# Kernel optimization log

Measured on AMD Instinct MI355X. Metric: run time of the kernel, lower is better.

The kernel has to match this reference:

```python
import jax, jax.numpy as jnp
import numpy as np

EPS = 1e-5  # BatchNorm eps; BN applied in eval mode with running_mean=0, running_var=1


def conv1x1(x, w, b=None):
    # x: [B,C,H,W], w: [O,C] -> [B,O,H,W]
    y = jnp.einsum('bchw,oc->bohw', x, w)
    if b is not None:
        y = y + b[None, :, None, None]
    return y


def bn_eval(x, gamma, beta):
    # running_mean=0, running_var=1
    scale = gamma / jnp.sqrt(1.0 + EPS)
    return x * scale[None, :, None, None] + beta[None, :, None, None]


def glnl_forward(x, mask, wt_nl, bt_nl, wp_nl, bp_nl, wt_l, bt_l, wp_l, bp_l,
                 wg_nl, bg_nl, wg_l, bg_l, wW, bW, gW, betaW, wWl, gWl, betaWl):
    B, C, H, W = x.shape
    I = wt_nl.shape[0]
    N = H * W

    # non-local branch score [B,N,N]
    th_nl = conv1x1(x, wt_nl, bt_nl).reshape(B, I, N)
    ph_nl = conv1x1(x, wp_nl, bp_nl).reshape(B, I, N)
    score_nl = jax.nn.softmax(jnp.einsum('bin,bim->bnm', th_nl, ph_nl), axis=-1)

    # local branch: mask-gated projections, score [B,N,N]
    m = mask.reshape(B, 1, N)
    th_l = conv1x1(x, wt_l, bt_l).reshape(B, I, N) * m
    ph_l = conv1x1(x, wp_l, bp_l).reshape(B, I, N) * m
    score_l = jax.nn.softmax(jnp.einsum('bin,bim->bnm', th_l, ph_l), axis=-1)

    # value projections [B,I,N]
    g_nl = conv1x1(x, wg_nl, bg_nl).reshape(B, I, N)
    g_l = conv1x1(x, wg_l, bg_l).reshape(B, I, N)

    # attention aggregation -> [B,I,H,W]
    y_nl = jnp.einsum('bnm,bim->bin', score_nl, g_nl).reshape(B, I, H, W)
    y_l = jnp.einsum('bnm,bim->bin', score_l, g_l).reshape(B, I, H, W)

    # W_local: conv1x1 (no bias) -> ReLU -> BN
    y_l = bn_eval(jax.nn.relu(conv1x1(y_l, wWl)), gWl, betaWl)

    y = y_nl + y_l
    # W: conv1x1 -> ReLU -> BN, then residual
    W_y = bn_eval(jax.nn.relu(conv1x1(y, wW, bW)), gW, betaW)
    return W_y + x


def setup_inputs() -> dict:
    key = jax.random.key(0)
    ks = jax.random.split(key, 20)
    B, C, I, H, W = 4, 128, 64, 64, 64
    s = 0.02
    inp = {
        'x': jax.random.normal(ks[0], (B, C, H, W), jnp.float32),
        'mask': (jax.random.uniform(ks[1], (B, 1, H, W)) > 0.5).astype(jnp.float32),
        'wt_nl': jax.random.normal(ks[2], (I, C)) * s, 'bt_nl': jnp.zeros((I,)),
        'wp_nl': jax.random.normal(ks[3], (I, C)) * s, 'bp_nl': jnp.zeros((I,)),
        'wt_l': jax.random.normal(ks[4], (I, C)) * s, 'bt_l': jnp.zeros((I,)),
        'wp_l': jax.random.normal(ks[5], (I, C)) * s, 'bp_l': jnp.zeros((I,)),
        'wg_nl': jax.random.normal(ks[6], (I, C)) * s, 'bg_nl': jnp.zeros((I,)),
        'wg_l': jax.random.normal(ks[7], (I, C)) * s, 'bg_l': jnp.zeros((I,)),
        'wW': jax.random.normal(ks[8], (C, I)) * s, 'bW': jnp.zeros((C,)),
        'gW': jnp.ones((C,)), 'betaW': jnp.zeros((C,)),
        'wWl': jax.random.normal(ks[9], (I, I)) * s,
        'gWl': jnp.ones((I,)), 'betaWl': jnp.zeros((I,)),
    }
    return inp


def reference(x, mask, wt_nl, bt_nl, wp_nl, bp_nl, wt_l, bt_l, wp_l, bp_l,
              wg_nl, bg_nl, wg_l, bg_l, wW, bW, gW, betaW, wWl, gWl, betaWl):
    return glnl_forward(x, mask, wt_nl, bt_nl, wp_nl, bp_nl, wt_l, bt_l, wp_l, bp_l,
                        wg_nl, bg_nl, wg_l, bg_l, wW, bW, gW, betaW, wWl, gWl, betaWl)
```

## Files before the change

kernel.cpp:

```cpp
#include <hip/hip_runtime.h>

typedef unsigned short u16;
typedef __attribute__((ext_vector_type(8))) short short8;
typedef __attribute__((ext_vector_type(4))) float floatx4;
typedef __attribute__((ext_vector_type(2))) unsigned int uint2e;

#define MFMA16(a, b, c) __builtin_amdgcn_mfma_f32_16x16x32_bf16((a), (b), (c), 0, 0, 0)
#define LOG2E 1.44269504088896340736f

#define SZ_P ((size_t)4 * 64 * 4096)

__device__ __forceinline__ float bf2f(u16 u) {
    union { unsigned int i; float f; } v; v.i = ((unsigned int)u) << 16; return v.f;
}
__device__ __forceinline__ u16 f2bf(float f) {
    union { float f; unsigned int i; } v; v.f = f;
    unsigned int r = v.i + 0x7fffu + ((v.i >> 16) & 1u);
    return (u16)(r >> 16);
}
__device__ __forceinline__ unsigned int cvtpk(float a, float b) {
    unsigned int r;
    asm("v_cvt_pk_bf16_f32 %0, %1, %2" : "=v"(r) : "v"(a), "v"(b));
    return r;
}
__device__ __forceinline__ void plswap32(unsigned int &a, unsigned int &b) {
#if __has_builtin(__builtin_amdgcn_permlane32_swap)
    uint2e r = __builtin_amdgcn_permlane32_swap(a, b, false, false);
    a = r.x; b = r.y;
#else
    asm volatile("v_permlane32_swap_b32 %0, %1" : "+v"(a), "+v"(b));
#endif
}
__device__ __forceinline__ void plswap16(unsigned int &a, unsigned int &b) {
#if __has_builtin(__builtin_amdgcn_permlane16_swap)
    uint2e r = __builtin_amdgcn_permlane16_swap(a, b, false, false);
    a = r.x; b = r.y;
#else
    asm volatile("v_permlane16_swap_b32 %0, %1" : "+v"(a), "+v"(b));
#endif
}
__device__ __forceinline__ int swz(int row, int g) {
    return row * 64 + (((g ^ (row & 7)) << 3));
}
__device__ __forceinline__ void gload16(const void* g, void* l) {
    __builtin_amdgcn_global_load_lds(
        (const __attribute__((address_space(1))) unsigned char*)g,
        (__attribute__((address_space(3))) unsigned char*)l, 16, 0, 0);
}

__global__ __launch_bounds__(256) void k_prep_w(
    const float* __restrict__ w0, const float* __restrict__ w1,
    const float* __restrict__ w2, const float* __restrict__ w3,
    const float* __restrict__ w4, const float* __restrict__ w5,
    const float* __restrict__ wWl, const float* __restrict__ wW,
    u16* __restrict__ wbf)
{
    const int idx = blockIdx.x * 256 + threadIdx.x;
    float v;
    if (idx < 49152) {
        const int j = idx >> 13, off = idx & 8191;
        const float* s = (j == 0) ? w0 : (j == 1) ? w1 : (j == 2) ? w2
                       : (j == 3) ? w3 : (j == 4) ? w4 : w5;
        v = s[off];
    } else if (idx < 53248) {
        v = wWl[idx - 49152];
    } else {
        v = wW[idx - 53248];
    }
    wbf[idx] = f2bf(v);
}

__global__ __launch_bounds__(256) void k_proj(
    const float* __restrict__ x, const float* __restrict__ mask,
    const u16* __restrict__ wbf,
    const float* __restrict__ bq0f, const float* __restrict__ bk0f,
    const float* __restrict__ bv0f,
    const float* __restrict__ bq1f, const float* __restrict__ bk1f,
    const float* __restrict__ bv1f,
    u16* __restrict__ q0, u16* __restrict__ k0, u16* __restrict__ v0,
    u16* __restrict__ q1, u16* __restrict__ k1, u16* __restrict__ v1)
{
    __shared__ __align__(16) u16 xt_s[64 * 136];
    const int n0 = blockIdx.x * 64, b = blockIdx.y;
    const int br = blockIdx.z;
    const u16* wq = wbf + br * 24576;
    const u16* wk = wq + 8192;
    const u16* wv = wk + 8192;
    const float* bq = br ? bq1f : bq0f;
    const float* bk = br ? bk1f : bk0f;
    const float* bv = br ? bv1f : bv0f;
    u16* q = br ? q1 : q0;  u16* k = br ? k1 : k0;  u16* v = br ? v1 : v0;

    const int t = threadIdx.x, w = t >> 6, lane = t & 63;
    const int quad = lane >> 4, l15 = lane & 15;
    const float* xb = x + ((size_t)b << 19);

    for (int idx = t; idx < 8192; idx += 256) {
        const int c = idx >> 6, n = idx & 63;
        xt_s[n * 136 + c] = f2bf(xb[((size_t)c << 12) + n0 + n]);
    }
    __syncthreads();

    short8 ax[4];
#pragma unroll
    for (int cc = 0; cc < 4; ++cc)
        ax[cc] = *(const short8*)&xt_s[(w * 16 + l15) * 136 + quad * 8 + cc * 32];

    float mv[4] = {1.f, 1.f, 1.f, 1.f};
    if (br) {
#pragma unroll
        for (int r = 0; r < 4; ++r)
            mv[r] = mask[((size_t)b << 12) + n0 + w * 16 + quad * 4 + r];
    }

#pragma unroll
    for (int qk = 0; qk < 2; ++qk) {
        const u16* wsel = qk ? wk : wq;
        const float* bb = qk ? bk : bq;
        u16* o = qk ? k : q;
        const float qscale = qk ? 1.0f : LOG2E;
#pragma unroll
        for (int ns = 0; ns < 4; ++ns) {
            floatx4 acc = {0.f, 0.f, 0.f, 0.f};
            const u16* wp = wsel + (ns * 16 + l15) * 128 + quad * 8;
#pragma unroll
            for (int cc = 0; cc < 4; ++cc)
                acc = MFMA16(ax[cc], *(const short8*)(wp + cc * 32), acc);
            const float bias_i = bb[ns * 16 + l15];
#pragma unroll
            for (int r = 0; r < 4; ++r) {
                const float val = (acc[r] + bias_i) * mv[r] * qscale;
                o[((size_t)b << 18) + (size_t)(n0 + w * 16 + quad * 4 + r) * 64
                  + ns * 16 + l15] = f2bf(val);
            }
        }
    }

    short8 aw[4];
#pragma unroll
    for (int cc = 0; cc < 4; ++cc)
        aw[cc] = *(const short8*)(wv + (w * 16 + l15) * 128 + quad * 8 + cc * 32);
    float bvr[4];
#pragma unroll
    for (int r = 0; r < 4; ++r) bvr[r] = bv[w * 16 + quad * 4 + r];
#pragma unroll
    for (int ns = 0; ns < 4; ++ns) {
        floatx4 acc = {0.f, 0.f, 0.f, 0.f};
#pragma unroll
        for (int cc = 0; cc < 4; ++cc)
            acc = MFMA16(aw[cc],
                *(const short8*)&xt_s[(ns * 16 + l15) * 136 + quad * 8 + cc * 32], acc);
#pragma unroll
        for (int r = 0; r < 4; ++r) {
            v[((size_t)b << 18) + ((size_t)(w * 16 + quad * 4 + r) << 12)
              + n0 + ns * 16 + l15] = f2bf(acc[r] + bvr[r]);
        }
    }
}

template<int NSP>
__global__ __launch_bounds__(512, 4) void k_flash(
    const u16* __restrict__ Q0, const u16* __restrict__ K0,
    const u16* __restrict__ V0,
    const u16* __restrict__ Q1, const u16* __restrict__ K1,
    const u16* __restrict__ V1,
    u16* __restrict__ num, float* __restrict__ den)
{
    constexpr int NIT = 4096 / NSP / 64;
    constexpr int SPB = (NSP == 4) ? 2 : 3;

    __shared__ __align__(16) u16 smem[18432];

    const int flat = blockIdx.x;
    const int g = flat & ((1 << (SPB + 3)) - 1), tile = flat >> (SPB + 3);
    const int b = g >> (SPB + 1), br = (g >> SPB) & 1, sp = g & (NSP - 1);
    const int z = br * NSP + sp;
    const int qb = tile * 256;
    const size_t base = ((size_t)b << 18);
    const u16* Q = (br ? Q1 : Q0) + base;
    const u16* K = (br ? K1 : K0) + base;
    const u16* V = (br ? V1 : V0) + base;
    u16* numo = num + (size_t)z * SZ_P + base;
    float* deno = den + z * 16384 + b * 4096;

    const int t = threadIdx.x, w = t >> 6, lane = t & 63;
    const int quad = lane >> 4, l15 = lane & 15;
    const int pw = w * 32 * 72;

    const int r0 = t >> 3;
    const int gx = (t & 7) ^ ((t >> 3) & 7);
    const u16* Kp0 = K + (size_t)r0 * 64 + gx * 8;
    const u16* Vp0 = V + ((size_t)r0 << 12) + gx * 8;
    u16* kw = smem + w * 512;
    u16* vw = smem + 8192 + w * 512;

    short8 aq[2][2];
#pragma unroll
    for (int t2 = 0; t2 < 2; ++t2)
#pragma unroll
        for (int s = 0; s < 2; ++s)
            aq[t2][s] = *(const short8*)(Q + (size_t)(qb + w * 32 + t2 * 16 + l15) * 64
                                         + s * 32 + quad * 8);

    floatx4 oacc[4][2];
#pragma unroll
    for (int it = 0; it < 4; ++it)
#pragma unroll
        for (int t2 = 0; t2 < 2; ++t2) oacc[it][t2] = (floatx4){0.f, 0.f, 0.f, 0.f};
    float dacc[2] = {0.f, 0.f};

    const int roff = tile & (NIT - 1);
    const int m_beg = sp * (4096 / NSP);

    {
        const int m0 = m_beg + (roff << 6);
        gload16(Kp0 + (size_t)m0 * 64, kw);
        gload16(Vp0 + m0, vw);
    }

    for (int j = 0; j < NIT; ++j) {
        const int cur = j & 1;
        asm volatile("s_waitcnt vmcnt(0)" ::: "memory");
        __builtin_amdgcn_sched_barrier(0);
        __syncthreads();
        if (j + 1 < NIT) {
            const int mn = m_beg + (((roff + j + 1) & (NIT - 1)) << 6);
            gload16(Kp0 + (size_t)mn * 64, kw + (cur ^ 1) * 4096);
            gload16(Vp0 + mn, vw + (cur ^ 1) * 4096);
        }
        const u16* kt = smem + cur * 4096;
        const u16* vt = smem + 8192 + cur * 4096;

#pragma unroll
        for (int s = 0; s < 2; ++s) {
            unsigned int w0[2][2], w1[2][2];
#pragma unroll
            for (int mtl = 0; mtl < 2; ++mtl) {
                const int mt = s * 2 + mtl;
                const int ko = swz(mt * 16 + l15, quad);
                const short8 ka0 = *(const short8*)(kt + ko);
                const short8 ka1 = *(const short8*)(kt + (ko ^ 32));
#pragma unroll
                for (int t2 = 0; t2 < 2; ++t2) {
                    floatx4 acc = {0.f, 0.f, 0.f, 0.f};
                    __builtin_amdgcn_s_setprio(1);
                    acc = MFMA16(ka0, aq[t2][0], acc);
                    acc = MFMA16(ka1, aq[t2][1], acc);
                    __builtin_amdgcn_s_setprio(0);
                    const float e0 = __builtin_amdgcn_exp2f(acc[0]);
                    const float e1 = __builtin_amdgcn_exp2f(acc[1]);
                    const float e2 = __builtin_amdgcn_exp2f(acc[2]);
                    const float e3 = __builtin_amdgcn_exp2f(acc[3]);
                    dacc[t2] += (e0 + e1) + (e2 + e3);
                    w0[mtl][t2] = cvtpk(e0, e1);
                    w1[mtl][t2] = cvtpk(e2, e3);
                }
            }
            short8 pb[2];
#pragma unroll
            for (int t2 = 0; t2 < 2; ++t2) {
                unsigned int a0 = w0[0][t2], b0 = w0[1][t2];
                unsigned int a1 = w1[0][t2], b1 = w1[1][t2];
                plswap32(a0, b0); plswap16(a0, b0);
                plswap32(a1, b1); plswap16(a1, b1);
                union { unsigned int u[4]; short8 s8; } cv;
                cv.u[0] = a0; cv.u[1] = a1; cv.u[2] = b0; cv.u[3] = b1;
                pb[t2] = cv.s8;
            }
            __builtin_amdgcn_s_setprio(1);
#pragma unroll
            for (int it = 0; it < 4; ++it) {
                const short8 va = *(const short8*)(vt + swz(it * 16 + l15, s * 4 + quad));
#pragma unroll
                for (int t2 = 0; t2 < 2; ++t2)
                    oacc[it][t2] = MFMA16(va, pb[t2], oacc[it][t2]);
            }
            __builtin_amdgcn_s_setprio(0);
        }
    }

#pragma unroll
    for (int t2 = 0; t2 < 2; ++t2) {
        float d = dacc[t2];
        d += __shfl_xor(d, 16, 64);
        d += __shfl_xor(d, 32, 64);
        if (quad == 0) deno[qb + w * 32 + t2 * 16 + l15] = d;
    }

    __syncthreads();
#pragma unroll
    for (int it = 0; it < 4; ++it)
#pragma unroll
        for (int t2 = 0; t2 < 2; ++t2) {
            *(uint2*)&smem[pw + (t2 * 16 + l15) * 72 + it * 16 + quad * 4] =
                make_uint2(cvtpk(oacc[it][t2][0], oacc[it][t2][1]),
                           cvtpk(oacc[it][t2][2], oacc[it][t2][3]));
        }
    __syncthreads();
#pragma unroll
    for (int ch = t; ch < 2048; ch += 512) {
        const int row = ch >> 3, cg = ch & 7;
        *(short8*)(numo + (size_t)(qb + row) * 64 + cg * 8) =
            *(const short8*)&smem[(row >> 5) * 2304 + (row & 31) * 72 + cg * 8];
    }
}

template<int NSP>
__global__ __launch_bounds__(256) void k_epi(
    const u16* __restrict__ num, const float* __restrict__ den,
    const u16* __restrict__ wbf,
    const float* __restrict__ gWl, const float* __restrict__ betaWl,
    const float* __restrict__ bW, const float* __restrict__ gW,
    const float* __restrict__ betaW,
    const float* __restrict__ x, float* __restrict__ out)
{
    __shared__ __align__(16) u16 yl_s[32 * 72];
    __shared__ __align__(16) u16 ynl_s[32 * 72];
    __shared__ __align__(16) u16 yy_s[32 * 72];
    const int b = blockIdx.y, n0 = blockIdx.x * 32;
    const int t = threadIdx.x, w = t >> 6, lane = t & 63;
    const int quad = lane >> 4, l15 = lane & 15;
    const size_t ybase = ((size_t)b << 18) + (size_t)n0 * 64;

    {
        const int row = t >> 3, cg = t & 7;
        float dn = 0.f, dl = 0.f;
#pragma unroll
        for (int sp = 0; sp < NSP; ++sp) {
            dn += den[sp * 16384 + b * 4096 + n0 + row];
            dl += den[(NSP + sp) * 16384 + b * 4096 + n0 + row];
        }
        const float inl = 1.0f / dn, ilo = 1.0f / dl;
        float an[8] = {0, 0, 0, 0, 0, 0, 0, 0}, al[8] = {0, 0, 0, 0, 0, 0, 0, 0};
#pragma unroll
        for (int sp = 0; sp < NSP; ++sp) {
            const short8 vn = *(const short8*)(num + (size_t)sp * SZ_P + ybase + row * 64 + cg * 8);
            const short8 vl = *(const short8*)(num + (size_t)(NSP + sp) * SZ_P + ybase + row * 64 + cg * 8);
#pragma unroll
            for (int j = 0; j < 8; ++j) {
                an[j] += bf2f((u16)vn[j]);
                al[j] += bf2f((u16)vl[j]);
            }
        }
        short8 ynl8, yl8;
#pragma unroll
        for (int j = 0; j < 8; ++j) {
            ynl8[j] = (short)f2bf(an[j] * inl);
            yl8[j]  = (short)f2bf(al[j] * ilo);
        }
        *(short8*)&ynl_s[row * 72 + cg * 8] = ynl8;
        *(short8*)&yl_s[row * 72 + cg * 8] = yl8;
    }
    __syncthreads();
    const float rsq = rsqrtf(1.0f + 1e-5f);
    const u16* wblW = wbf + 49152;
    const u16* wbW  = wbf + 53248;

    {
        const short8 a0 = *(const short8*)(wblW + (w * 16 + l15) * 64 + quad * 8);
        const short8 a1 = *(const short8*)(wblW + (w * 16 + l15) * 64 + 32 + quad * 8);
        float sc[4], bt[4];
#pragma unroll
        for (int r = 0; r < 4; ++r) {
            const int io = w * 16 + quad * 4 + r;
            sc[r] = gWl[io] * rsq;
            bt[r] = betaWl[io];
        }
#pragma unroll
        for (int nh = 0; nh < 2; ++nh) {
            floatx4 acc = {0.f, 0.f, 0.f, 0.f};
            const u16* bp_ = &yl_s[(nh * 16 + l15) * 72 + quad * 8];
            acc = MFMA16(a0, *(const short8*)bp_, acc);
            acc = MFMA16(a1, *(const short8*)(bp_ + 32), acc);
#pragma unroll
            for (int r = 0; r < 4; ++r) {
                const int io = w * 16 + quad * 4 + r;
                float val = fmaxf(acc[r], 0.f) * sc[r] + bt[r];
                val += bf2f(ynl_s[(nh * 16 + l15) * 72 + io]);
                yy_s[(nh * 16 + l15) * 72 + io] = f2bf(val);
            }
        }
    }
    __syncthreads();

#pragma unroll
    for (int rb = 0; rb < 2; ++rb) {
        const int c0 = rb * 64 + w * 16;
        const short8 a0 = *(const short8*)(wbW + (c0 + l15) * 64 + quad * 8);
        const short8 a1 = *(const short8*)(wbW + (c0 + l15) * 64 + 32 + quad * 8);
        float bs[4], sc[4], bt[4];
#pragma unroll
        for (int r = 0; r < 4; ++r) {
            const int c = c0 + quad * 4 + r;
            bs[r] = bW[c];
            sc[r] = gW[c] * rsq;
            bt[r] = betaW[c];
        }
#pragma unroll
        for (int nh = 0; nh < 2; ++nh) {
            floatx4 acc = {0.f, 0.f, 0.f, 0.f};
            const u16* bp_ = &yy_s[(nh * 16 + l15) * 72 + quad * 8];
            acc = MFMA16(a0, *(const short8*)bp_, acc);
            acc = MFMA16(a1, *(const short8*)(bp_ + 32), acc);
#pragma unroll
            for (int r = 0; r < 4; ++r) {
                const int c = c0 + quad * 4 + r;
                float val = fmaxf(acc[r] + bs[r], 0.f) * sc[r] + bt[r];
                const size_t xi = ((size_t)b << 19) + ((size_t)c << 12) + n0 + nh * 16 + l15;
                out[xi] = val + x[xi];
            }
        }
    }
}

extern "C" void kernel_launch(void* const* d_in, const int* in_sizes, int n_in,
                              void* d_out, int out_size, void* d_ws, size_t ws_size,
                              hipStream_t stream) {
    const float* x      = (const float*)d_in[0];
    const float* mask   = (const float*)d_in[1];
    const float* wt_nl  = (const float*)d_in[2];  const float* bt_nl = (const float*)d_in[3];
    const float* wp_nl  = (const float*)d_in[4];  const float* bp_nl = (const float*)d_in[5];
    const float* wt_l   = (const float*)d_in[6];  const float* bt_l  = (const float*)d_in[7];
    const float* wp_l   = (const float*)d_in[8];  const float* bp_l  = (const float*)d_in[9];
    const float* wg_nl  = (const float*)d_in[10]; const float* bg_nl = (const float*)d_in[11];
    const float* wg_l   = (const float*)d_in[12]; const float* bg_l  = (const float*)d_in[13];
    const float* wW     = (const float*)d_in[14]; const float* bW    = (const float*)d_in[15];
    const float* gW     = (const float*)d_in[16]; const float* betaW = (const float*)d_in[17];
    const float* wWl    = (const float*)d_in[18]; const float* gWl   = (const float*)d_in[19];
    const float* betaWl = (const float*)d_in[20];

    const size_t need8 = ((size_t)61440 + 6 * SZ_P + 16 * SZ_P) * 2
                       + (size_t)16 * 16384 * 4;
    const int nsp = (ws_size >= need8) ? 8 : 4;

    u16* ws  = (u16*)d_ws;
    u16* wbf = ws;
    u16* q0  = wbf + 61440;
    u16* k0  = q0 + SZ_P;
    u16* v0  = k0 + SZ_P;
    u16* q1  = v0 + SZ_P;
    u16* k1  = q1 + SZ_P;
    u16* v1  = k1 + SZ_P;
    u16* num = v1 + SZ_P;
    float* den = (float*)(num + (size_t)2 * nsp * SZ_P);

    k_prep_w<<<dim3(240), 256, 0, stream>>>(wt_nl, wp_nl, wg_nl,
                                            wt_l, wp_l, wg_l, wWl, wW, wbf);
    k_proj<<<dim3(64, 4, 2), 256, 0, stream>>>(x, mask, wbf,
        bt_nl, bp_nl, bg_nl, bt_l, bp_l, bg_l,
        q0, k0, v0, q1, k1, v1);
    if (nsp == 8) {
        k_flash<8><<<dim3(1024), 512, 0, stream>>>(q0, k0, v0, q1, k1, v1, num, den);
        k_epi<8><<<dim3(128, 4), 256, 0, stream>>>(num, den, wbf, gWl, betaWl,
                                                   bW, gW, betaW, x, (float*)d_out);
    } else {
        k_flash<4><<<dim3(512), 512, 0, stream>>>(q0, k0, v0, q1, k1, v1, num, den);
        k_epi<4><<<dim3(128, 4), 256, 0, stream>>>(num, den, wbf, gWl, betaWl,
                                                   bW, gW, betaW, x, (float*)d_out);
    }
}
```

Measured before the change: 166.5 us.

## Fuse both branches in projection, fix split-K at 4, compute denominators via MFMA

The projection kernel now computes both the non-local and local branches in one block, so the x tile is staged in LDS once instead of twice. The flash kernel is fixed to a 4-way key split, removing the 8-way path that the old code picked when the workspace was large enough. Softmax row sums now come from an extra MFMA against a ones vector instead of scalar adds plus cross-lane shuffles. Risks: fewer projection blocks, less parallelism in the flash kernel, and bf16-rounded probabilities in the denominator.

```diff
diff --git a/kernel.cpp b/kernel.cpp
--- a/kernel.cpp
+++ b/kernel.cpp
@@ -9,6 +9,7 @@
 #define LOG2E 1.44269504088896340736f
 
 #define SZ_P ((size_t)4 * 64 * 4096)
+#define NSP 4
 
 __device__ __forceinline__ float bf2f(u16 u) {
     union { unsigned int i; float f; } v; v.i = ((unsigned int)u) << 16; return v.f;
@@ -82,14 +83,6 @@
 {
     __shared__ __align__(16) u16 xt_s[64 * 136];
     const int n0 = blockIdx.x * 64, b = blockIdx.y;
-    const int br = blockIdx.z;
-    const u16* wq = wbf + br * 24576;
-    const u16* wk = wq + 8192;
-    const u16* wv = wk + 8192;
-    const float* bq = br ? bq1f : bq0f;
-    const float* bk = br ? bk1f : bk0f;
-    const float* bv = br ? bv1f : bv0f;
-    u16* q = br ? q1 : q0;  u16* k = br ? k1 : k0;  u16* v = br ? v1 : v0;
 
     const int t = threadIdx.x, w = t >> 6, lane = t & 63;
     const int quad = lane >> 4, l15 = lane & 15;
@@ -106,59 +99,69 @@
     for (int cc = 0; cc < 4; ++cc)
         ax[cc] = *(const short8*)&xt_s[(w * 16 + l15) * 136 + quad * 8 + cc * 32];
 
-    float mv[4] = {1.f, 1.f, 1.f, 1.f};
-    if (br) {
-#pragma unroll
-        for (int r = 0; r < 4; ++r)
-            mv[r] = mask[((size_t)b << 12) + n0 + w * 16 + quad * 4 + r];
-    }
-
-#pragma unroll
-    for (int qk = 0; qk < 2; ++qk) {
-        const u16* wsel = qk ? wk : wq;
-        const float* bb = qk ? bk : bq;
-        u16* o = qk ? k : q;
-        const float qscale = qk ? 1.0f : LOG2E;
+#pragma unroll
+    for (int br = 0; br < 2; ++br) {
+        const u16* wq = wbf + br * 24576;
+        const u16* wk = wq + 8192;
+        const u16* wv = wk + 8192;
+        const float* bq = br ? bq1f : bq0f;
+        const float* bk = br ? bk1f : bk0f;
+        const float* bv = br ? bv1f : bv0f;
+        u16* q = br ? q1 : q0;  u16* k = br ? k1 : k0;  u16* v = br ? v1 : v0;
+
+        float mv[4] = {1.f, 1.f, 1.f, 1.f};
+        if (br) {
+#pragma unroll
+            for (int r = 0; r < 4; ++r)
+                mv[r] = mask[((size_t)b << 12) + n0 + w * 16 + quad * 4 + r];
+        }
+
+#pragma unroll
+        for (int qk = 0; qk < 2; ++qk) {
+            const u16* wsel = qk ? wk : wq;
+            const float* bb = qk ? bk : bq;
+            u16* o = qk ? k : q;
+            const float qscale = qk ? 1.0f : LOG2E;
+#pragma unroll
+            for (int ns = 0; ns < 4; ++ns) {
+                floatx4 acc = {0.f, 0.f, 0.f, 0.f};
+                const u16* wp = wsel + (ns * 16 + l15) * 128 + quad * 8;
+#pragma unroll
+                for (int cc = 0; cc < 4; ++cc)
+                    acc = MFMA16(ax[cc], *(const short8*)(wp + cc * 32), acc);
+                const float bias_i = bb[ns * 16 + l15];
+#pragma unroll
+                for (int r = 0; r < 4; ++r) {
+                    const float val = (acc[r] + bias_i) * mv[r] * qscale;
+                    o[((size_t)b << 18) + (size_t)(n0 + w * 16 + quad * 4 + r) * 64
+                      + ns * 16 + l15] = f2bf(val);
+                }
+            }
+        }
+
+        short8 aw[4];
+#pragma unroll
+        for (int cc = 0; cc < 4; ++cc)
+            aw[cc] = *(const short8*)(wv + (w * 16 + l15) * 128 + quad * 8 + cc * 32);
+        float bvr[4];
+#pragma unroll
+        for (int r = 0; r < 4; ++r) bvr[r] = bv[w * 16 + quad * 4 + r];
 #pragma unroll
         for (int ns = 0; ns < 4; ++ns) {
             floatx4 acc = {0.f, 0.f, 0.f, 0.f};
-            const u16* wp = wsel + (ns * 16 + l15) * 128 + quad * 8;
 #pragma unroll
             for (int cc = 0; cc < 4; ++cc)
-                acc = MFMA16(ax[cc], *(const short8*)(wp + cc * 32), acc);
-            const float bias_i = bb[ns * 16 + l15];
+                acc = MFMA16(aw[cc],
+                    *(const short8*)&xt_s[(ns * 16 + l15) * 136 + quad * 8 + cc * 32], acc);
 #pragma unroll
             for (int r = 0; r < 4; ++r) {
-                const float val = (acc[r] + bias_i) * mv[r] * qscale;
-                o[((size_t)b << 18) + (size_t)(n0 + w * 16 + quad * 4 + r) * 64
-                  + ns * 16 + l15] = f2bf(val);
-            }
-        }
-    }
-
-    short8 aw[4];
-#pragma unroll
-    for (int cc = 0; cc < 4; ++cc)
-        aw[cc] = *(const short8*)(wv + (w * 16 + l15) * 128 + quad * 8 + cc * 32);
-    float bvr[4];
-#pragma unroll
-    for (int r = 0; r < 4; ++r) bvr[r] = bv[w * 16 + quad * 4 + r];
-#pragma unroll
-    for (int ns = 0; ns < 4; ++ns) {
-        floatx4 acc = {0.f, 0.f, 0.f, 0.f};
-#pragma unroll
-        for (int cc = 0; cc < 4; ++cc)
-            acc = MFMA16(aw[cc],
-                *(const short8*)&xt_s[(ns * 16 + l15) * 136 + quad * 8 + cc * 32], acc);
-#pragma unroll
-        for (int r = 0; r < 4; ++r) {
-            v[((size_t)b << 18) + ((size_t)(w * 16 + quad * 4 + r) << 12)
-              + n0 + ns * 16 + l15] = f2bf(acc[r] + bvr[r]);
-        }
-    }
-}
-
-template<int NSP>
+                v[((size_t)b << 18) + ((size_t)(w * 16 + quad * 4 + r) << 12)
+                  + n0 + ns * 16 + l15] = f2bf(acc[r] + bvr[r]);
+            }
+        }
+    }
+}
+
 __global__ __launch_bounds__(512, 4) void k_flash(
     const u16* __restrict__ Q0, const u16* __restrict__ K0,
     const u16* __restrict__ V0,
@@ -167,13 +170,12 @@
     u16* __restrict__ num, float* __restrict__ den)
 {
     constexpr int NIT = 4096 / NSP / 64;
-    constexpr int SPB = (NSP == 4) ? 2 : 3;
 
     __shared__ __align__(16) u16 smem[18432];
 
     const int flat = blockIdx.x;
-    const int g = flat & ((1 << (SPB + 3)) - 1), tile = flat >> (SPB + 3);
-    const int b = g >> (SPB + 1), br = (g >> SPB) & 1, sp = g & (NSP - 1);
+    const int g = flat & 31, tile = flat >> 5;
+    const int b = g >> 3, br = (g >> 2) & 1, sp = g & 3;
     const int z = br * NSP + sp;
     const int qb = tile * 256;
     const size_t base = ((size_t)b << 18);
@@ -207,7 +209,11 @@
     for (int it = 0; it < 4; ++it)
 #pragma unroll
         for (int t2 = 0; t2 < 2; ++t2) oacc[it][t2] = (floatx4){0.f, 0.f, 0.f, 0.f};
-    float dacc[2] = {0.f, 0.f};
+    floatx4 dacc4[2];
+    dacc4[0] = (floatx4){0.f, 0.f, 0.f, 0.f};
+    dacc4[1] = (floatx4){0.f, 0.f, 0.f, 0.f};
+    const short8 vone = {(short)0x3F80, (short)0x3F80, (short)0x3F80, (short)0x3F80,
+                         (short)0x3F80, (short)0x3F80, (short)0x3F80, (short)0x3F80};
 
     const int roff = tile & (NIT - 1);
     const int m_beg = sp * (4096 / NSP);
@@ -251,7 +257,6 @@
                     const float e1 = __builtin_amdgcn_exp2f(acc[1]);
                     const float e2 = __builtin_amdgcn_exp2f(acc[2]);
                     const float e3 = __builtin_amdgcn_exp2f(acc[3]);
-                    dacc[t2] += (e0 + e1) + (e2 + e3);
                     w0[mtl][t2] = cvtpk(e0, e1);
                     w1[mtl][t2] = cvtpk(e2, e3);
                 }
@@ -275,16 +280,16 @@
                 for (int t2 = 0; t2 < 2; ++t2)
                     oacc[it][t2] = MFMA16(va, pb[t2], oacc[it][t2]);
             }
+            dacc4[0] = MFMA16(vone, pb[0], dacc4[0]);
+            dacc4[1] = MFMA16(vone, pb[1], dacc4[1]);
             __builtin_amdgcn_s_setprio(0);
         }
     }
 
-#pragma unroll
-    for (int t2 = 0; t2 < 2; ++t2) {
-        float d = dacc[t2];
-        d += __shfl_xor(d, 16, 64);
-        d += __shfl_xor(d, 32, 64);
-        if (quad == 0) deno[qb + w * 32 + t2 * 16 + l15] = d;
+    if (quad == 0) {
+#pragma unroll
+        for (int t2 = 0; t2 < 2; ++t2)
+            deno[qb + w * 32 + t2 * 16 + l15] = dacc4[t2][0];
     }
 
     __syncthreads();
@@ -305,7 +310,6 @@
     }
 }
 
-template<int NSP>
 __global__ __launch_bounds__(256) void k_epi(
     const u16* __restrict__ num, const float* __restrict__ den,
     const u16* __restrict__ wbf,
@@ -429,10 +433,6 @@
     const float* wWl    = (const float*)d_in[18]; const float* gWl   = (const float*)d_in[19];
     const float* betaWl = (const float*)d_in[20];
 
-    const size_t need8 = ((size_t)61440 + 6 * SZ_P + 16 * SZ_P) * 2
-                       + (size_t)16 * 16384 * 4;
-    const int nsp = (ws_size >= need8) ? 8 : 4;
-
     u16* ws  = (u16*)d_ws;
     u16* wbf = ws;
     u16* q0  = wbf + 61440;
@@ -442,20 +442,14 @@
     u16* k1  = q1 + SZ_P;
     u16* v1  = k1 + SZ_P;
     u16* num = v1 + SZ_P;
-    float* den = (float*)(num + (size_t)2 * nsp * SZ_P);
+    float* den = (float*)(num + (size_t)2 * NSP * SZ_P);
 
     k_prep_w<<<dim3(240), 256, 0, stream>>>(wt_nl, wp_nl, wg_nl,
                                             wt_l, wp_l, wg_l, wWl, wW, wbf);
-    k_proj<<<dim3(64, 4, 2), 256, 0, stream>>>(x, mask, wbf,
+    k_proj<<<dim3(64, 4), 256, 0, stream>>>(x, mask, wbf,
         bt_nl, bp_nl, bg_nl, bt_l, bp_l, bg_l,
         q0, k0, v0, q1, k1, v1);
-    if (nsp == 8) {
-        k_flash<8><<<dim3(1024), 512, 0, stream>>>(q0, k0, v0, q1, k1, v1, num, den);
-        k_epi<8><<<dim3(128, 4), 256, 0, stream>>>(num, den, wbf, gWl, betaWl,
-                                                   bW, gW, betaW, x, (float*)d_out);
-    } else {
-        k_flash<4><<<dim3(512), 512, 0, stream>>>(q0, k0, v0, q1, k1, v1, num, den);
-        k_epi<4><<<dim3(128, 4), 256, 0, stream>>>(num, den, wbf, gWl, betaWl,
-                                                   bW, gW, betaW, x, (float*)d_out);
-    }
-}
+    k_flash<<<dim3(512), 512, 0, stream>>>(q0, k0, v0, q1, k1, v1, num, den);
+    k_epi<<<dim3(128, 4), 256, 0, stream>>>(num, den, wbf, gWl, betaWl,
+                                            bW, gW, betaW, x, (float*)d_out);
+}
```

Measured after the change: 166.3 us. Within noise of the previous version (-0.1%).
